# Optimization experiments

Hardware: AMD Instinct MI355X
Metric: run time of the kernel (lower is better)

## Reference

```python
import jax, jax.numpy as jnp
import numpy as np


def setup_inputs() -> dict:
    key = jax.random.key(0)
    kq, kk, kv = jax.random.split(key, 3)
    B, N, H, D = 1, 4096, 16, 64
    q = jax.random.normal(kq, (B, N, H, D), dtype=jnp.float32)
    k = jax.random.normal(kk, (B, N, H, D), dtype=jnp.float32)
    v = jax.random.normal(kv, (B, N, H, D), dtype=jnp.float32)
    return {"q": q, "k": k, "v": v}


def reference(q, k, v):
    # q, k, v: [b, n, h, d]
    d = q.shape[-1]
    scale = 1.0 / jnp.sqrt(jnp.asarray(d, dtype=q.dtype))
    # scores: [b, h, n_q, n_k]
    scores = jnp.einsum("bqhd,bkhd->bhqk", q, k) * scale
    attn = jax.nn.softmax(scores, axis=-1)
    # output back in [b, n, h, d] layout
    out = jnp.einsum("bhqk,bkhd->bqhd", attn, v)
    return out
```

## Files before the change

### kernel.cpp

```cpp
#include <hip/hip_runtime.h>
#include <hip/hip_bf16.h>

#define H 16
#define D 64
#define NSEQ 4096
#define BM 128
#define BN 64
#define NT (NSEQ / BN)

typedef __attribute__((ext_vector_type(8))) short bf16x8;
typedef __attribute__((ext_vector_type(4))) short short4v;
typedef __attribute__((ext_vector_type(4))) float f32x4;
typedef __attribute__((ext_vector_type(4))) float f4v;

union BF8 { bf16x8 v; unsigned u[4]; };
union S4  { short4v s; unsigned u[2]; };

static __device__ __forceinline__ unsigned pk2(float lo, float hi) {
    __hip_bfloat162 h = __float22bfloat162_rn(float2{lo, hi});
    unsigned u;
    __builtin_memcpy(&u, &h, 4);
    return u;
}

static __device__ __forceinline__ float fexp2(float x) {
#if __has_builtin(__builtin_amdgcn_exp2f)
    return __builtin_amdgcn_exp2f(x);
#else
    return exp2f(x);
#endif
}

#define TO_GBL(p) ((const __attribute__((address_space(1))) int*)(unsigned long long)(p))
#define TO_LDS(p) ((__attribute__((address_space(3))) int*)(unsigned int)(unsigned long long)(p))

__global__ void prep(const float* __restrict__ k, const float* __restrict__ v,
                     short* __restrict__ kb, short* __restrict__ vt) {
    __shared__ short L[64 * 72];
    const int h = blockIdx.y, n0 = blockIdx.x * 64, t = threadIdx.x;
    const int rw = t >> 4, c4 = (t & 15) * 4;
    #pragma unroll
    for (int it = 0; it < 4; ++it) {
        const int row = rw + it * 16;
        const size_t gro = ((size_t)(n0 + row) * H + h) * D + c4;
        f4v kf = *(const f4v*)(k + gro);
        S4 ks;
        ks.u[0] = pk2(kf[0], kf[1]);
        ks.u[1] = pk2(kf[2], kf[3]);
        *(short4v*)(kb + ((size_t)h * NSEQ + n0 + row) * D + c4) = ks.s;

        f4v vf = *(const f4v*)(v + gro);
        S4 vs;
        vs.u[0] = pk2(vf[0], vf[1]);
        vs.u[1] = pk2(vf[2], vf[3]);
        *(short4v*)&L[row * 72 + c4] = vs.s;
    }
    __syncthreads();
    const int tr = t & 15, tc = t >> 4;
    const int r0 = tr * 4, d0 = tc * 4;
    short4v ra[4];
    #pragma unroll
    for (int i = 0; i < 4; ++i) {
        const int s = r0 + i, s32 = s & 31, base32 = (s >> 5) * 32;
        const int phys = base32 + ((s32 >> 3) * 4 + (s32 & 3) + 16 * ((s32 >> 2) & 1));
        ra[i] = *(const short4v*)&L[phys * 72 + d0];
    }
    #pragma unroll
    for (int jj = 0; jj < 4; ++jj) {
        short4v o4 = (short4v){ra[0][jj], ra[1][jj], ra[2][jj], ra[3][jj]};
        *(short4v*)(vt + ((size_t)(h * D + d0 + jj)) * NSEQ + n0 + r0) = o4;
    }
}

__global__ __launch_bounds__(128, 1)
void attn_fwd(const float* __restrict__ q, const short* __restrict__ kb,
              const short* __restrict__ vtb, float* __restrict__ out)
{
    const int lin   = blockIdx.x;
    const int idx   = lin >> 3;
    const int h     = (lin & 7) * 2 + (idx >> 5);
    const int qbase = (idx & 31) * BM;

    const int tid   = threadIdx.x;
    const int wave  = tid >> 6;
    const int lane  = tid & 63;
    const int lm    = lane & 15;
    const int quad  = lane >> 4;
    const int sw    = lm & 7;

    __shared__ short Kt[4][BN * D];
    __shared__ short Vt[4][BN * D];

    const float c1 = 0.18033688011112042f;

    bf16x8 bq[4][2];
    #pragma unroll
    for (int g = 0; g < 4; ++g) {
        const int qrow = qbase + wave * 64 + g * 16 + lm;
        #pragma unroll
        for (int kc = 0; kc < 2; ++kc) {
            const float* qp = q + ((size_t)qrow * H + h) * D + kc * 32 + quad * 8;
            f4v q0 = *(const f4v*)qp;
            f4v q1 = *(const f4v*)(qp + 4);
            BF8 b;
            b.u[0] = pk2(q0[0] * c1, q0[1] * c1); b.u[1] = pk2(q0[2] * c1, q0[3] * c1);
            b.u[2] = pk2(q1[0] * c1, q1[1] * c1); b.u[3] = pk2(q1[2] * c1, q1[3] * c1);
            bq[g][kc] = b.v;
        }
    }

    BF8 ones;
    ones.u[0] = ones.u[1] = ones.u[2] = ones.u[3] = 0x3F803F80u;

    const f32x4 fz = (f32x4){0.f, 0.f, 0.f, 0.f};
    f32x4 o[4][4];
    #pragma unroll
    for (int g = 0; g < 4; ++g)
        #pragma unroll
        for (int mb = 0; mb < 4; ++mb) o[g][mb] = fz;
    f32x4 lacc[4];
    lacc[0] = fz; lacc[1] = fz; lacc[2] = fz; lacc[3] = fz;

    const int cset = wave * 4;
    const int ciA = (cset + 0) * 64 + lane;
    const int ciB = (cset + 1) * 64 + lane;
    const int ciC = (cset + 2) * 64 + lane;
    const int ciD = (cset + 3) * 64 + lane;
    const int krA = ciA >> 3, kpA = (ciA & 7) ^ (krA & 7);
    const int krB = ciB >> 3, kpB = (ciB & 7) ^ (krB & 7);
    const int krC = ciC >> 3, kpC = (ciC & 7) ^ (krC & 7);
    const int krD = ciD >> 3, kpD = (ciD & 7) ^ (krD & 7);

    const short* kh = kb  + (size_t)h * NSEQ * D;
    const short* vh = vtb + (size_t)h * D * NSEQ;
    const short* pkA = kh + (size_t)krA * D + kpA * 8;
    const short* pkB = kh + (size_t)krB * D + kpB * 8;
    const short* pkC = kh + (size_t)krC * D + kpC * 8;
    const short* pkD = kh + (size_t)krD * D + kpD * 8;
    const short* pvA = vh + (size_t)krA * NSEQ + kpA * 8;
    const short* pvB = vh + (size_t)krB * NSEQ + kpB * 8;
    const short* pvC = vh + (size_t)krC * NSEQ + kpC * 8;
    const short* pvD = vh + (size_t)krD * NSEQ + kpD * 8;

    auto issue = [&](int b) {
        __builtin_amdgcn_global_load_lds(TO_GBL(pkA), TO_LDS(&Kt[b][(cset + 0) * 512]), 16, 0, 0);
        __builtin_amdgcn_global_load_lds(TO_GBL(pkB), TO_LDS(&Kt[b][(cset + 1) * 512]), 16, 0, 0);
        __builtin_amdgcn_global_load_lds(TO_GBL(pkC), TO_LDS(&Kt[b][(cset + 2) * 512]), 16, 0, 0);
        __builtin_amdgcn_global_load_lds(TO_GBL(pkD), TO_LDS(&Kt[b][(cset + 3) * 512]), 16, 0, 0);
        __builtin_amdgcn_global_load_lds(TO_GBL(pvA), TO_LDS(&Vt[b][(cset + 0) * 512]), 16, 0, 0);
        __builtin_amdgcn_global_load_lds(TO_GBL(pvB), TO_LDS(&Vt[b][(cset + 1) * 512]), 16, 0, 0);
        __builtin_amdgcn_global_load_lds(TO_GBL(pvC), TO_LDS(&Vt[b][(cset + 2) * 512]), 16, 0, 0);
        __builtin_amdgcn_global_load_lds(TO_GBL(pvD), TO_LDS(&Vt[b][(cset + 3) * 512]), 16, 0, 0);
        pkA += BN * D; pkB += BN * D; pkC += BN * D; pkD += BN * D;
        pvA += BN; pvB += BN; pvC += BN; pvD += BN;
    };

    const int posK0 = ((0 + quad) ^ sw) * 8;
    const int posK1 = ((4 + quad) ^ sw) * 8;

    auto compute = [&](int b) {
        const short* K_ = Kt[b];
        const short* V_ = Vt[b];

        bf16x8 kf0[4], kf1[4];
        #pragma unroll
        for (int nb = 0; nb < 4; ++nb) {
            kf0[nb] = *(const bf16x8*)&K_[(nb * 16 + lm) * 64 + posK0];
            kf1[nb] = *(const bf16x8*)&K_[(nb * 16 + lm) * 64 + posK1];
        }

        BF8 pb[4][2];
        #pragma unroll
        for (int g = 0; g < 4; ++g) {
            f32x4 st[4];
            #pragma unroll
            for (int nb = 0; nb < 4; ++nb) {
                st[nb] = __builtin_amdgcn_mfma_f32_16x16x32_bf16(kf0[nb], bq[g][0], fz, 0, 0, 0);
                st[nb] = __builtin_amdgcn_mfma_f32_16x16x32_bf16(kf1[nb], bq[g][1], st[nb], 0, 0, 0);
            }
            #pragma unroll
            for (int nb = 0; nb < 4; ++nb)
                #pragma unroll
                for (int r = 0; r < 4; ++r)
                    st[nb][r] = fexp2(st[nb][r]);
            #pragma unroll
            for (int c = 0; c < 2; ++c) {
                pb[g][c].u[0] = pk2(st[2 * c][0],     st[2 * c][1]);
                pb[g][c].u[1] = pk2(st[2 * c][2],     st[2 * c][3]);
                pb[g][c].u[2] = pk2(st[2 * c + 1][0], st[2 * c + 1][1]);
                pb[g][c].u[3] = pk2(st[2 * c + 1][2], st[2 * c + 1][3]);
            }
        }

        #pragma unroll
        for (int c = 0; c < 2; ++c)
            #pragma unroll
            for (int g = 0; g < 4; ++g)
                lacc[g] = __builtin_amdgcn_mfma_f32_16x16x32_bf16(ones.v, pb[g][c].v, lacc[g], 0, 0, 0);

        #pragma unroll
        for (int c = 0; c < 2; ++c) {
            const int pos = ((c * 4 + quad) ^ sw) * 8;
            #pragma unroll
            for (int mb = 0; mb < 4; ++mb) {
                bf16x8 vf = *(const bf16x8*)&V_[(mb * 16 + lm) * 64 + pos];
                #pragma unroll
                for (int g = 0; g < 4; ++g)
                    o[g][mb] = __builtin_amdgcn_mfma_f32_16x16x32_bf16(vf, pb[g][c].v, o[g][mb], 0, 0, 0);
            }
        }
    };

#define WAITV0 asm volatile("s_waitcnt vmcnt(0)" ::: "memory")
#define BARRIER() do { __builtin_amdgcn_s_barrier(); asm volatile("" ::: "memory"); } while (0)

    issue(0); issue(1);

    for (int k = 0; k < 15; ++k) {
        WAITV0; BARRIER();
        issue(2); issue(3);
        compute(0); compute(1);
        WAITV0; BARRIER();
        issue(0); issue(1);
        compute(2); compute(3);
    }
    WAITV0; BARRIER();
    issue(2); issue(3);
    compute(0); compute(1);
    WAITV0; BARRIER();
    compute(2); compute(3);

    #pragma unroll
    for (int g = 0; g < 4; ++g) {
        const float inv = 1.0f / lacc[g][0];
        const int qrow = qbase + wave * 64 + g * 16 + lm;
        float* op = out + ((size_t)qrow * H + h) * D + quad * 4;
        #pragma unroll
        for (int mb = 0; mb < 4; ++mb) {
            f4v w;
            #pragma unroll
            for (int r = 0; r < 4; ++r) w[r] = o[g][mb][r] * inv;
            *(f4v*)(op + mb * 16) = w;
        }
    }
}

extern "C" void kernel_launch(void* const* d_in, const int* in_sizes, int n_in,
                              void* d_out, int out_size, void* d_ws, size_t ws_size,
                              hipStream_t stream) {
    const float* q = (const float*)d_in[0];
    const float* k = (const float*)d_in[1];
    const float* v = (const float*)d_in[2];
    float* out = (float*)d_out;

    short* kb = (short*)d_ws;
    short* vt = kb + (size_t)H * NSEQ * D;

    prep<<<dim3(NSEQ / 64, H), dim3(256), 0, stream>>>(k, v, kb, vt);
    attn_fwd<<<dim3((NSEQ / BM) * H), dim3(128), 0, stream>>>(q, kb, vt, out);
}
```

Baseline: 179.2 us.

## Split key range across two wave groups per block and merge in LDS

The Q tile doubles to 256 rows and blocks grow to 8 waves. Four query groups are each processed by two wave groups, and each wave group covers half of the key/value sequence with its own double-buffered LDS tiles. Partial outputs and row sums from the second half are combined through LDS before the normalized store. The aim is more waves per CU for better latency hiding and MFMA utilization. In exchange it doubles LDS use, adds a reduction step with extra barriers, and the tighter launch bounds risk register pressure or spilling.

```diff
diff --git a/kernel.cpp b/kernel.cpp
--- a/kernel.cpp
+++ b/kernel.cpp
@@ -4,9 +4,10 @@
 #define H 16
 #define D 64
 #define NSEQ 4096
-#define BM 128
+#define BM 256
 #define BN 64
 #define NT (NSEQ / BN)
+#define NTH (NT / 2)
 
 typedef __attribute__((ext_vector_type(8))) short bf16x8;
 typedef __attribute__((ext_vector_type(4))) short short4v;
@@ -72,31 +73,34 @@
     }
 }
 
-__global__ __launch_bounds__(128, 1)
+__global__ __launch_bounds__(512, 2)
 void attn_fwd(const float* __restrict__ q, const short* __restrict__ kb,
               const short* __restrict__ vtb, float* __restrict__ out)
 {
     const int lin   = blockIdx.x;
     const int idx   = lin >> 3;
-    const int h     = (lin & 7) * 2 + (idx >> 5);
-    const int qbase = (idx & 31) * BM;
+    const int h     = (lin & 7) * 2 + (idx >> 4);
+    const int qbase = (idx & 15) * BM;
 
     const int tid   = threadIdx.x;
     const int wave  = tid >> 6;
+    const int kg    = wave >> 2;
+    const int qg    = wave & 3;
     const int lane  = tid & 63;
     const int lm    = lane & 15;
     const int quad  = lane >> 4;
     const int sw    = lm & 7;
-
-    __shared__ short Kt[4][BN * D];
-    __shared__ short Vt[4][BN * D];
+    const int T0    = kg * NTH;
+
+    __shared__ short Kt[2][4][BN * D];
+    __shared__ short Vt[2][4][BN * D];
 
     const float c1 = 0.18033688011112042f;
 
     bf16x8 bq[4][2];
     #pragma unroll
     for (int g = 0; g < 4; ++g) {
-        const int qrow = qbase + wave * 64 + g * 16 + lm;
+        const int qrow = qbase + qg * 64 + g * 16 + lm;
         #pragma unroll
         for (int kc = 0; kc < 2; ++kc) {
             const float* qp = q + ((size_t)qrow * H + h) * D + kc * 32 + quad * 8;
@@ -121,46 +125,32 @@
     f32x4 lacc[4];
     lacc[0] = fz; lacc[1] = fz; lacc[2] = fz; lacc[3] = fz;
 
-    const int cset = wave * 4;
-    const int ciA = (cset + 0) * 64 + lane;
-    const int ciB = (cset + 1) * 64 + lane;
-    const int ciC = (cset + 2) * 64 + lane;
-    const int ciD = (cset + 3) * 64 + lane;
-    const int krA = ciA >> 3, kpA = (ciA & 7) ^ (krA & 7);
-    const int krB = ciB >> 3, kpB = (ciB & 7) ^ (krB & 7);
-    const int krC = ciC >> 3, kpC = (ciC & 7) ^ (krC & 7);
-    const int krD = ciD >> 3, kpD = (ciD & 7) ^ (krD & 7);
+    const int ci0 = (qg * 2 + 0) * 64 + lane;
+    const int ci1 = (qg * 2 + 1) * 64 + lane;
+    const int kr0 = ci0 >> 3, kp0 = (ci0 & 7) ^ (kr0 & 7);
+    const int kr1 = ci1 >> 3, kp1 = (ci1 & 7) ^ (kr1 & 7);
 
     const short* kh = kb  + (size_t)h * NSEQ * D;
     const short* vh = vtb + (size_t)h * D * NSEQ;
-    const short* pkA = kh + (size_t)krA * D + kpA * 8;
-    const short* pkB = kh + (size_t)krB * D + kpB * 8;
-    const short* pkC = kh + (size_t)krC * D + kpC * 8;
-    const short* pkD = kh + (size_t)krD * D + kpD * 8;
-    const short* pvA = vh + (size_t)krA * NSEQ + kpA * 8;
-    const short* pvB = vh + (size_t)krB * NSEQ + kpB * 8;
-    const short* pvC = vh + (size_t)krC * NSEQ + kpC * 8;
-    const short* pvD = vh + (size_t)krD * NSEQ + kpD * 8;
+    const short* pkA = kh + (size_t)(T0 * BN + kr0) * D + kp0 * 8;
+    const short* pkB = kh + (size_t)(T0 * BN + kr1) * D + kp1 * 8;
+    const short* pvA = vh + (size_t)kr0 * NSEQ + T0 * BN + kp0 * 8;
+    const short* pvB = vh + (size_t)kr1 * NSEQ + T0 * BN + kp1 * 8;
 
     auto issue = [&](int b) {
-        __builtin_amdgcn_global_load_lds(TO_GBL(pkA), TO_LDS(&Kt[b][(cset + 0) * 512]), 16, 0, 0);
-        __builtin_amdgcn_global_load_lds(TO_GBL(pkB), TO_LDS(&Kt[b][(cset + 1) * 512]), 16, 0, 0);
-        __builtin_amdgcn_global_load_lds(TO_GBL(pkC), TO_LDS(&Kt[b][(cset + 2) * 512]), 16, 0, 0);
-        __builtin_amdgcn_global_load_lds(TO_GBL(pkD), TO_LDS(&Kt[b][(cset + 3) * 512]), 16, 0, 0);
-        __builtin_amdgcn_global_load_lds(TO_GBL(pvA), TO_LDS(&Vt[b][(cset + 0) * 512]), 16, 0, 0);
-        __builtin_amdgcn_global_load_lds(TO_GBL(pvB), TO_LDS(&Vt[b][(cset + 1) * 512]), 16, 0, 0);
-        __builtin_amdgcn_global_load_lds(TO_GBL(pvC), TO_LDS(&Vt[b][(cset + 2) * 512]), 16, 0, 0);
-        __builtin_amdgcn_global_load_lds(TO_GBL(pvD), TO_LDS(&Vt[b][(cset + 3) * 512]), 16, 0, 0);
-        pkA += BN * D; pkB += BN * D; pkC += BN * D; pkD += BN * D;
-        pvA += BN; pvB += BN; pvC += BN; pvD += BN;
+        __builtin_amdgcn_global_load_lds(TO_GBL(pkA), TO_LDS(&Kt[kg][b][(qg * 2 + 0) * 512]), 16, 0, 0);
+        __builtin_amdgcn_global_load_lds(TO_GBL(pkB), TO_LDS(&Kt[kg][b][(qg * 2 + 1) * 512]), 16, 0, 0);
+        __builtin_amdgcn_global_load_lds(TO_GBL(pvA), TO_LDS(&Vt[kg][b][(qg * 2 + 0) * 512]), 16, 0, 0);
+        __builtin_amdgcn_global_load_lds(TO_GBL(pvB), TO_LDS(&Vt[kg][b][(qg * 2 + 1) * 512]), 16, 0, 0);
+        pkA += BN * D; pkB += BN * D; pvA += BN; pvB += BN;
     };
 
     const int posK0 = ((0 + quad) ^ sw) * 8;
     const int posK1 = ((4 + quad) ^ sw) * 8;
 
     auto compute = [&](int b) {
-        const short* K_ = Kt[b];
-        const short* V_ = Vt[b];
+        const short* K_ = Kt[kg][b];
+        const short* V_ = Vt[kg][b];
 
         bf16x8 kf0[4], kf1[4];
         #pragma unroll
@@ -216,7 +206,7 @@
 
     issue(0); issue(1);
 
-    for (int k = 0; k < 15; ++k) {
+    for (int k = 0; k < 7; ++k) {
         WAITV0; BARRIER();
         issue(2); issue(3);
         compute(0); compute(1);
@@ -230,17 +220,41 @@
     WAITV0; BARRIER();
     compute(2); compute(3);
 
-    #pragma unroll
-    for (int g = 0; g < 4; ++g) {
-        const float inv = 1.0f / lacc[g][0];
-        const int qrow = qbase + wave * 64 + g * 16 + lm;
-        float* op = out + ((size_t)qrow * H + h) * D + quad * 4;
-        #pragma unroll
-        for (int mb = 0; mb < 4; ++mb) {
-            f4v w;
-            #pragma unroll
-            for (int r = 0; r < 4; ++r) w[r] = o[g][mb][r] * inv;
-            *(f4v*)(op + mb * 16) = w;
+    float* Mo = (float*)&Kt[0][0][0];
+    float* Ml = (float*)&Vt[0][0][0];
+    const int slot = qg * 64 + lane;
+
+    __syncthreads();
+    if (kg == 1) {
+        float* p = Mo + slot * 64;
+        #pragma unroll
+        for (int g = 0; g < 4; ++g)
+            #pragma unroll
+            for (int mb = 0; mb < 4; ++mb) {
+                const int fi = g * 4 + mb;
+                *(f32x4*)(p + ((fi ^ (slot & 15)) * 4)) = o[g][mb];
+            }
+        f32x4 lv = (f32x4){lacc[0][0], lacc[1][0], lacc[2][0], lacc[3][0]};
+        *(f32x4*)(Ml + slot * 4) = lv;
+    }
+    __syncthreads();
+    if (kg == 0) {
+        const float* p = Mo + slot * 64;
+        const f32x4 lv = *(const f32x4*)(Ml + slot * 4);
+        #pragma unroll
+        for (int g = 0; g < 4; ++g) {
+            const float inv = 1.0f / (lacc[g][0] + lv[g]);
+            const int qrow = qbase + qg * 64 + g * 16 + lm;
+            float* op = out + ((size_t)qrow * H + h) * D + quad * 4;
+            #pragma unroll
+            for (int mb = 0; mb < 4; ++mb) {
+                const int fi = g * 4 + mb;
+                const f32x4 ob = *(const f32x4*)(p + ((fi ^ (slot & 15)) * 4));
+                f4v w;
+                #pragma unroll
+                for (int r = 0; r < 4; ++r) w[r] = (o[g][mb][r] + ob[r]) * inv;
+                *(f4v*)(op + mb * 16) = w;
+            }
         }
     }
 }
@@ -257,5 +271,5 @@
     short* vt = kb + (size_t)H * NSEQ * D;
 
     prep<<<dim3(NSEQ / 64, H), dim3(256), 0, stream>>>(k, v, kb, vt);
-    attn_fwd<<<dim3((NSEQ / BM) * H), dim3(128), 0, stream>>>(q, kb, vt, out);
-}
+    attn_fwd<<<dim3((NSEQ / BM) * H * 2 / 2), dim3(512), 0, stream>>>(q, kb, vt, out);
+}
```

Result: faster. 163.4 us (-8.8%).
